# Optimization experiments

Hardware: AMD Instinct MI355X
Metric: run time of the kernel (lower is better)

## Reference

```python
import jax, jax.numpy as jnp
import numpy as np

N = 100000   # nodes
E = 1600000  # edges (avg degree 16)
H = 4        # heads
D = 32       # per-head dim (= output_dim)
IN = 32      # input_dim (== output_dim for residual)
NEG_SLOPE = 0.2  # DGL GATConv leaky_relu default


def setup_inputs() -> dict:
    key = jax.random.key(0)
    ks = jax.random.split(key, 9)
    h = jax.random.normal(ks[0], (N, IN), jnp.float32)
    src = jax.random.randint(ks[1], (E,), 0, N, jnp.int32)
    dst = jax.random.randint(ks[2], (E,), 0, N, jnp.int32)
    W_fc = jax.random.normal(ks[3], (IN, H * D), jnp.float32) / np.sqrt(IN).astype(np.float32)
    attn_l = jax.random.normal(ks[4], (H, D), jnp.float32) * 0.1
    attn_r = jax.random.normal(ks[5], (H, D), jnp.float32) * 0.1
    bias_gat = jnp.zeros((H * D,), jnp.float32)
    W_out = jax.random.normal(ks[6], (H * D, D), jnp.float32) / np.sqrt(H * D).astype(np.float32)
    b_out = jnp.zeros((D,), jnp.float32)
    return {"h": h, "src": src, "dst": dst, "W_fc": W_fc, "attn_l": attn_l,
            "attn_r": attn_r, "bias_gat": bias_gat, "W_out": W_out, "b_out": b_out}


def reference(h, src, dst, W_fc, attn_l, attn_r, bias_gat, W_out, b_out):
    # GATConv: linear projection to [N, H, D]
    feat = (h @ W_fc).reshape(N, H, D)
    el = jnp.einsum('nhd,hd->nh', feat, attn_l)  # [N,H]
    er = jnp.einsum('nhd,hd->nh', feat, attn_r)  # [N,H]
    # per-edge unnormalized score, leaky relu
    e = el[src] + er[dst]                         # [E,H]
    e = jnp.where(e > 0, e, NEG_SLOPE * e)
    # segment softmax over edges grouped by destination node
    emax = jax.ops.segment_max(e, dst, num_segments=N)            # [N,H]
    ex = jnp.exp(e - emax[dst])                                   # [E,H]
    denom = jax.ops.segment_sum(ex, dst, num_segments=N)         # [N,H]
    alpha = ex / jnp.maximum(denom[dst], 1e-9)                    # [E,H]
    # attention-weighted scatter-add aggregation
    msg = feat[src] * alpha[:, :, None]                           # [E,H,D]
    rst = jax.ops.segment_sum(msg, dst, num_segments=N)          # [N,H,D]
    rst = rst.reshape(N, H * D) + bias_gat
    # out projection + ELU activation + residual
    out = rst @ W_out + b_out
    out = jnp.where(out > 0, out, jnp.expm1(out))  # ELU(alpha=1)
    return h + out
```

## Files before the change

### kernel.cpp

```cpp
#include <hip/hip_runtime.h>
#include <hip/hip_bf16.h>

#define NNODE 100000
#define NEDGE 1600000
#define NBLK_SCAN 98
#define HIST_BLOCKS 512
#define PROJ_BLOCKS 1563
#define FLAGBIT 0x80000000u

static __device__ __forceinline__ uint32_t pack_bf16(float a, float b) {
    __hip_bfloat162 t = __float22bfloat162_rn(make_float2(a, b));
    return *(uint32_t*)&t;
}

__global__ __launch_bounds__(256) void k_proj_hist(
        const float* __restrict__ hin, const float* __restrict__ Wfc,
        const float* __restrict__ attn_l, const float* __restrict__ attn_r,
        uint32_t* __restrict__ feat, float* __restrict__ el, float* __restrict__ er,
        const int* __restrict__ dst, int* __restrict__ cnt, int* __restrict__ pos) {
    __shared__ float sW[32 * 128];
    __shared__ float sh[64 * 32];
    int tid = threadIdx.x;
    if (blockIdx.x < HIST_BLOCKS) {
        int i = blockIdx.x * 256 + tid;
        const int4* d4 = (const int4*)dst;
        int4* p4 = (int4*)pos;
        for (int e = i; e < NEDGE / 4; e += HIST_BLOCKS * 256) {
            int4 d = d4[e];
            int4 p;
            p.x = atomicAdd(&cnt[d.x], 1);
            p.y = atomicAdd(&cnt[d.y], 1);
            p.z = atomicAdd(&cnt[d.z], 1);
            p.w = atomicAdd(&cnt[d.w], 1);
            p4[e] = p;
        }
        return;
    }
    int nbase = (blockIdx.x - HIST_BLOCKS) * 64;
    for (int i = tid * 4; i < 4096; i += 256 * 4)
        *(float4*)&sW[i] = *(const float4*)&Wfc[i];
    for (int i = tid * 4; i < 2048; i += 1024) {
        int n = nbase + (i >> 5);
        float4 v = make_float4(0.f, 0.f, 0.f, 0.f);
        if (n < NNODE) v = *(const float4*)&hin[n * 32 + (i & 31)];
        *(float4*)&sh[i] = v;
    }
    __syncthreads();
    int nl = tid >> 2, hh = tid & 3;
    int n = nbase + nl;
    float acc[32];
#pragma unroll
    for (int d = 0; d < 32; d++) acc[d] = 0.f;
#pragma unroll 8
    for (int k = 0; k < 32; k++) {
        float hk = sh[nl * 32 + k];
#pragma unroll
        for (int d = 0; d < 32; d++)
            acc[d] = fmaf(hk, sW[k * 128 + hh * 32 + d], acc[d]);
    }
    if (n < NNODE) {
        float e_l = 0.f, e_r = 0.f;
#pragma unroll
        for (int d = 0; d < 32; d++) {
            e_l = fmaf(acc[d], attn_l[hh * 32 + d], e_l);
            e_r = fmaf(acc[d], attn_r[hh * 32 + d], e_r);
        }
        el[n * 4 + hh] = e_l;
        er[n * 4 + hh] = e_r;
        uint4 u[4];
#pragma unroll
        for (int q = 0; q < 4; q++) {
            u[q].x = pack_bf16(acc[q * 8 + 0], acc[q * 8 + 1]);
            u[q].y = pack_bf16(acc[q * 8 + 2], acc[q * 8 + 3]);
            u[q].z = pack_bf16(acc[q * 8 + 4], acc[q * 8 + 5]);
            u[q].w = pack_bf16(acc[q * 8 + 6], acc[q * 8 + 7]);
        }
#pragma unroll
        for (int q = 0; q < 4; q++)
            *(uint4*)&feat[(size_t)n * 64 + hh * 16 + q * 4] = u[q];
    }
}

__global__ __launch_bounds__(256) void k_scan(
        const int* __restrict__ cnt, unsigned* __restrict__ word,
        int* __restrict__ offa) {
    __shared__ int s[256];
    __shared__ int sBase;
    int t = threadIdx.x;
    int b = blockIdx.x;
    int base = b * 1024 + t * 4;
    int v[4];
#pragma unroll
    for (int i = 0; i < 4; i++) {
        int n = base + i;
        v[i] = (n < NNODE) ? cnt[n] : 0;
    }
    int sum = v[0] + v[1] + v[2] + v[3];
    s[t] = sum;
    __syncthreads();
    for (int d = 1; d < 256; d <<= 1) {
        int x = (t >= d) ? s[t - d] : 0;
        __syncthreads();
        s[t] += x;
        __syncthreads();
    }
    int excl = s[t] - sum;
    if (t == 255)
        __hip_atomic_store(&word[b], (unsigned)s[255] | FLAGBIT,
                           __ATOMIC_RELEASE, __HIP_MEMORY_SCOPE_AGENT);
    if (t < 64) {
        unsigned acc = 0;
        for (int i = t; i < b; i += 64) {
            unsigned w;
            do {
                w = __hip_atomic_load(&word[i], __ATOMIC_ACQUIRE, __HIP_MEMORY_SCOPE_AGENT);
            } while (!(w & FLAGBIT));
            acc += w & ~FLAGBIT;
        }
#pragma unroll
        for (int o = 32; o; o >>= 1) acc += __shfl_down(acc, o);
        if (t == 0) sBase = (int)acc;
    }
    __syncthreads();
    int o0 = sBase + excl;
#pragma unroll
    for (int i = 0; i < 4; i++) {
        int n = base + i;
        if (n < NNODE) { offa[n] = o0; o0 += v[i]; }
    }
    if (b == NBLK_SCAN - 1 && t == 255) offa[NNODE] = NEDGE;
}

__global__ __launch_bounds__(256) void k_scatter(const int* __restrict__ src,
                                                 const int* __restrict__ dst,
                                                 const int* __restrict__ pos,
                                                 const int* __restrict__ offa,
                                                 int* __restrict__ ssrc) {
    int i = blockIdx.x * 256 + threadIdx.x;
    if (i >= NEDGE / 4) return;
    int4 s = ((const int4*)src)[i];
    int4 d = ((const int4*)dst)[i];
    int4 p = ((const int4*)pos)[i];
    int o0 = offa[d.x];
    int o1 = offa[d.y];
    int o2 = offa[d.z];
    int o3 = offa[d.w];
    ssrc[o0 + p.x] = s.x;
    ssrc[o1 + p.y] = s.y;
    ssrc[o2 + p.z] = s.z;
    ssrc[o3 + p.w] = s.w;
}

#define NPB 4
union SmemU {
    struct { int sS[NPB][64]; float sE[NPB][64][4]; } g;
    struct { float sv[NPB][128]; float sacc[NPB][2][32]; } e;
};

__global__ __launch_bounds__(256) void k_gather(
        const int* __restrict__ off, const int* __restrict__ ssrc,
        const float* __restrict__ el, const float* __restrict__ er,
        const uint32_t* __restrict__ feat, const float* __restrict__ bias_gat,
        const float* __restrict__ Wout, const float* __restrict__ b_out,
        const float* __restrict__ hin, float* __restrict__ out) {
    __shared__ float sW[128 * 32];
    __shared__ __align__(16) SmemU U;
    int tid = threadIdx.x;
    for (int i = tid * 4; i < 4096; i += 1024)
        *(float4*)&sW[i] = *(const float4*)&Wout[i];
    int w = tid >> 6;
    int l = tid & 63;
    int n = blockIdx.x * NPB + w;
    int c0 = l * 2;
    int hh = l >> 4;
    float2 acc = make_float2(0.f, 0.f);
    float den = 0.f;
    int beg = off[n], end = off[n + 1];
    float4 erv = *(const float4*)&er[n * 4];

    for (int base = beg; base < end; base += 64) {
        int cnt = end - base; if (cnt > 64) cnt = 64;
        if (l < cnt) {
            int s = ssrc[base + l];
            float4 ev = *(const float4*)&el[s * 4];
            float4 e4;
            e4.x = ev.x + erv.x; e4.x = e4.x > 0.f ? e4.x : 0.2f * e4.x; e4.x = __expf(e4.x);
            e4.y = ev.y + erv.y; e4.y = e4.y > 0.f ? e4.y : 0.2f * e4.y; e4.y = __expf(e4.y);
            e4.z = ev.z + erv.z; e4.z = e4.z > 0.f ? e4.z : 0.2f * e4.z; e4.z = __expf(e4.z);
            e4.w = ev.w + erv.w; e4.w = e4.w > 0.f ? e4.w : 0.2f * e4.w; e4.w = __expf(e4.w);
            U.g.sS[w][l] = s;
            *(float4*)&U.g.sE[w][l][0] = e4;
        }
        __builtin_amdgcn_wave_barrier();
        int e = 0;
        for (; e + 8 <= cnt; e += 8) {
            int ss[8]; float xx[8]; uint32_t uu[8];
#pragma unroll
            for (int q = 0; q < 8; q++) {
                ss[q] = U.g.sS[w][e + q];
                xx[q] = U.g.sE[w][e + q][hh];
            }
#pragma unroll
            for (int q = 0; q < 8; q++)
                uu[q] = feat[(uint32_t)ss[q] * 64u + (uint32_t)l];
#pragma unroll
            for (int q = 0; q < 8; q++) {
                den += xx[q];
                acc.x = fmaf(xx[q], __uint_as_float(uu[q] << 16), acc.x);
                acc.y = fmaf(xx[q], __uint_as_float(uu[q] & 0xffff0000u), acc.y);
            }
        }
        for (; e < cnt; e++) {
            int s0 = U.g.sS[w][e];
            float x0 = U.g.sE[w][e][hh];
            uint32_t u0 = feat[(uint32_t)s0 * 64u + (uint32_t)l];
            den += x0;
            acc.x = fmaf(x0, __uint_as_float(u0 << 16), acc.x);
            acc.y = fmaf(x0, __uint_as_float(u0 & 0xffff0000u), acc.y);
        }
        __builtin_amdgcn_wave_barrier();
    }
    float inv = 1.f / fmaxf(den, 1e-9f);
    float2 val;
    val.x = acc.x * inv + bias_gat[c0];
    val.y = acc.y * inv + bias_gat[c0 + 1];
    __syncthreads();
    *(float2*)&U.e.sv[w][c0] = val;
    __syncthreads();
    int j = tid & 31, g2 = (l >> 5);
    float p = 0.f;
    const float* vv = U.e.sv[w];
#pragma unroll 16
    for (int cc = g2 * 64; cc < g2 * 64 + 64; cc++)
        p = fmaf(vv[cc], sW[cc * 32 + j], p);
    U.e.sacc[w][g2][j] = p;
    __syncthreads();
    if (g2 == 0) {
        float a = U.e.sacc[w][0][j] + U.e.sacc[w][1][j] + b_out[j];
        a = a > 0.f ? a : expm1f(a);
        out[n * 32 + j] = hin[n * 32 + j] + a;
    }
}

extern "C" void kernel_launch(void* const* d_in, const int* in_sizes, int n_in,
                              void* d_out, int out_size, void* d_ws, size_t ws_size,
                              hipStream_t stream) {
    const float* hin      = (const float*)d_in[0];
    const int*   src      = (const int*)d_in[1];
    const int*   dst      = (const int*)d_in[2];
    const float* Wfc      = (const float*)d_in[3];
    const float* attn_l   = (const float*)d_in[4];
    const float* attn_r   = (const float*)d_in[5];
    const float* bias_gat = (const float*)d_in[6];
    const float* Wout     = (const float*)d_in[7];
    const float* b_out    = (const float*)d_in[8];
    float* out = (float*)d_out;

    char* ws = (char*)d_ws;
    size_t o = 0;
    uint32_t* feat = (uint32_t*)(ws + o); o += (size_t)NNODE * 64 * 4;
    float* el      = (float*)(ws + o);    o += (size_t)NNODE * 4 * 4;
    float* er      = (float*)(ws + o);    o += (size_t)NNODE * 4 * 4;
    int*   cnt     = (int*)(ws + o);      o += (size_t)NNODE * 4;
    unsigned* word = (unsigned*)(ws + o); o += (size_t)NBLK_SCAN * 4;
    int*   offa    = (int*)(ws + o);      o += (size_t)(NNODE + 1) * 4;
    int*   pos     = (int*)(ws + o);      o += (size_t)NEDGE * 4;
    int*   ssrc    = (int*)(ws + o);      o += (size_t)NEDGE * 4;

    hipMemsetAsync(cnt, 0, (size_t)(NNODE + NBLK_SCAN) * 4, stream);

    k_proj_hist<<<HIST_BLOCKS + PROJ_BLOCKS, 256, 0, stream>>>(
        hin, Wfc, attn_l, attn_r, feat, el, er, dst, cnt, pos);
    k_scan<<<NBLK_SCAN, 256, 0, stream>>>(cnt, word, offa);
    k_scatter<<<(NEDGE / 4 + 255) / 256, 256, 0, stream>>>(src, dst, pos, offa, ssrc);
    k_gather<<<NNODE / NPB, 256, 0, stream>>>(offa, ssrc, el, er, feat, bias_gat,
                                              Wout, b_out, hin, out);
}
```

Baseline: 264.1 us.

## Restructure projection to keep W in registers, one node per wave iteration

Rewrites the fused projection kernel. Each lane now holds two output columns of W_fc in registers and loops over 64 nodes per wave, reading h rows through uniform broadcast loads instead of LDS. It computes el/er with a 16-lane shuffle reduction and writes the bf16 features coalesced. The histogram branch changes from a grid-stride loop to one int4 per thread, so block counts shift toward many more hist blocks and fewer projection blocks. This drops LDS use and the syncthreads, but loads of h are now repeated per lane.

```diff
diff --git a/kernel.cpp b/kernel.cpp
--- a/kernel.cpp
+++ b/kernel.cpp
@@ -4,8 +4,8 @@
 #define NNODE 100000
 #define NEDGE 1600000
 #define NBLK_SCAN 98
-#define HIST_BLOCKS 512
-#define PROJ_BLOCKS 1563
+#define HIST_BLOCKS 1563
+#define PROJ_BLOCKS 391
 #define FLAGBIT 0x80000000u
 
 static __device__ __forceinline__ uint32_t pack_bf16(float a, float b) {
@@ -18,66 +18,58 @@
         const float* __restrict__ attn_l, const float* __restrict__ attn_r,
         uint32_t* __restrict__ feat, float* __restrict__ el, float* __restrict__ er,
         const int* __restrict__ dst, int* __restrict__ cnt, int* __restrict__ pos) {
-    __shared__ float sW[32 * 128];
-    __shared__ float sh[64 * 32];
     int tid = threadIdx.x;
     if (blockIdx.x < HIST_BLOCKS) {
         int i = blockIdx.x * 256 + tid;
-        const int4* d4 = (const int4*)dst;
-        int4* p4 = (int4*)pos;
-        for (int e = i; e < NEDGE / 4; e += HIST_BLOCKS * 256) {
-            int4 d = d4[e];
+        if (i < NEDGE / 4) {
+            int4 d = ((const int4*)dst)[i];
             int4 p;
             p.x = atomicAdd(&cnt[d.x], 1);
             p.y = atomicAdd(&cnt[d.y], 1);
             p.z = atomicAdd(&cnt[d.z], 1);
             p.w = atomicAdd(&cnt[d.w], 1);
-            p4[e] = p;
+            ((int4*)pos)[i] = p;
         }
         return;
     }
-    int nbase = (blockIdx.x - HIST_BLOCKS) * 64;
-    for (int i = tid * 4; i < 4096; i += 256 * 4)
-        *(float4*)&sW[i] = *(const float4*)&Wfc[i];
-    for (int i = tid * 4; i < 2048; i += 1024) {
-        int n = nbase + (i >> 5);
-        float4 v = make_float4(0.f, 0.f, 0.f, 0.f);
-        if (n < NNODE) v = *(const float4*)&hin[n * 32 + (i & 31)];
-        *(float4*)&sh[i] = v;
-    }
-    __syncthreads();
-    int nl = tid >> 2, hh = tid & 3;
-    int n = nbase + nl;
-    float acc[32];
-#pragma unroll
-    for (int d = 0; d < 32; d++) acc[d] = 0.f;
-#pragma unroll 8
-    for (int k = 0; k < 32; k++) {
-        float hk = sh[nl * 32 + k];
-#pragma unroll
-        for (int d = 0; d < 32; d++)
-            acc[d] = fmaf(hk, sW[k * 128 + hh * 32 + d], acc[d]);
-    }
-    if (n < NNODE) {
-        float e_l = 0.f, e_r = 0.f;
-#pragma unroll
-        for (int d = 0; d < 32; d++) {
-            e_l = fmaf(acc[d], attn_l[hh * 32 + d], e_l);
-            e_r = fmaf(acc[d], attn_r[hh * 32 + d], e_r);
-        }
-        el[n * 4 + hh] = e_l;
-        er[n * 4 + hh] = e_r;
-        uint4 u[4];
-#pragma unroll
-        for (int q = 0; q < 4; q++) {
-            u[q].x = pack_bf16(acc[q * 8 + 0], acc[q * 8 + 1]);
-            u[q].y = pack_bf16(acc[q * 8 + 2], acc[q * 8 + 3]);
-            u[q].z = pack_bf16(acc[q * 8 + 4], acc[q * 8 + 5]);
-            u[q].w = pack_bf16(acc[q * 8 + 6], acc[q * 8 + 7]);
-        }
-#pragma unroll
-        for (int q = 0; q < 4; q++)
-            *(uint4*)&feat[(size_t)n * 64 + hh * 16 + q * 4] = u[q];
+    int l = tid & 63;
+    int w = tid >> 6;
+    int nbase = (blockIdx.x - HIST_BLOCKS) * 256 + w * 64;
+    int c0 = l * 2;
+    float2 wreg[32];
+#pragma unroll
+    for (int k = 0; k < 32; k++)
+        wreg[k] = *(const float2*)&Wfc[k * 128 + c0];
+    float al0 = attn_l[c0], al1 = attn_l[c0 + 1];
+    float ar0 = attn_r[c0], ar1 = attn_r[c0 + 1];
+#pragma unroll 2
+    for (int i = 0; i < 64; i++) {
+        int n = nbase + i;
+        if (n >= NNODE) break;
+        float4 hv[8];
+#pragma unroll
+        for (int j = 0; j < 8; j++)
+            hv[j] = *(const float4*)&hin[n * 32 + j * 4];
+        float a0 = 0.f, a1 = 0.f;
+#pragma unroll
+        for (int j = 0; j < 8; j++) {
+            a0 = fmaf(hv[j].x, wreg[j * 4 + 0].x, a0); a1 = fmaf(hv[j].x, wreg[j * 4 + 0].y, a1);
+            a0 = fmaf(hv[j].y, wreg[j * 4 + 1].x, a0); a1 = fmaf(hv[j].y, wreg[j * 4 + 1].y, a1);
+            a0 = fmaf(hv[j].z, wreg[j * 4 + 2].x, a0); a1 = fmaf(hv[j].z, wreg[j * 4 + 2].y, a1);
+            a0 = fmaf(hv[j].w, wreg[j * 4 + 3].x, a0); a1 = fmaf(hv[j].w, wreg[j * 4 + 3].y, a1);
+        }
+        float ep = a0 * al0 + a1 * al1;
+        float rp = a0 * ar0 + a1 * ar1;
+#pragma unroll
+        for (int m = 8; m; m >>= 1) {
+            ep += __shfl_xor(ep, m);
+            rp += __shfl_xor(rp, m);
+        }
+        if ((l & 15) == 0) {
+            el[n * 4 + (l >> 4)] = ep;
+            er[n * 4 + (l >> 4)] = rp;
+        }
+        feat[(size_t)n * 64 + l] = pack_bf16(a0, a1);
     }
 }
 
```

Result: slower. 274.5 us (+3.9%).
